# Kernel optimization log

Measured on AMD Instinct MI355X. Metric: run time of the kernel, lower is better.

Reference implementation:

```python
import jax, jax.numpy as jnp
import numpy as np

_SAMPLING_EPS = 1e-5


def setup_inputs() -> dict:
    key = jax.random.key(0)
    ks = jax.random.split(key, 7)
    N, V, H = 256, 128000, 200  # num_seqs, vocab_size, output-history length
    logits = jax.random.normal(ks[0], (N, V), dtype=jnp.float32)
    output_tokens = jax.random.randint(ks[1], (N, H), 0, V, dtype=jnp.int32)
    presence_penalties = jax.random.uniform(ks[2], (N,), jnp.float32, 0.0, 2.0)
    frequency_penalties = jax.random.uniform(ks[3], (N,), jnp.float32, 0.0, 2.0)
    temperatures = jax.random.uniform(ks[4], (N,), jnp.float32, 0.5, 1.5)
    top_ps = jax.random.uniform(ks[5], (N,), jnp.float32, 0.5, 1.0)
    top_ks = jax.random.randint(ks[6], (N,), 1, 1000, dtype=jnp.int32)
    return {
        "logits": logits,
        "presence_penalties": presence_penalties,
        "frequency_penalties": frequency_penalties,
        "temperatures": temperatures,
        "top_ps": top_ps,
        "output_tokens": output_tokens,
        "top_ks": top_ks,
    }


def reference(logits, presence_penalties, frequency_penalties, temperatures,
              top_ps, output_tokens, top_ks):
    N, V = logits.shape

    # ---- _apply_penalties: bincount of previously generated tokens per row ----
    rows = jnp.arange(N)[:, None]  # [N,1] broadcast against [N,H] token ids
    bin_counts = jnp.zeros((N, V), logits.dtype).at[rows, output_tokens].add(1.0)
    # rows are skipped when both penalties are < eps (original builds an index list)
    active = ((presence_penalties >= _SAMPLING_EPS) |
              (frequency_penalties >= _SAMPLING_EPS))[:, None]
    presence_mask = (bin_counts > 0.0).astype(logits.dtype)
    penalty = (frequency_penalties[:, None] * bin_counts
               + presence_penalties[:, None] * presence_mask)
    logits = logits - jnp.where(active, penalty, jnp.zeros((), logits.dtype))

    # ---- temperature scaling + softmax ----
    logits = logits / temperatures[:, None]
    probs = jax.nn.softmax(logits, axis=-1)

    # ---- _apply_top_p_top_k: sort desc, cumsum, mask, unsort ----
    probs_idx = jnp.argsort(-probs, axis=-1)                    # descending order
    probs_sort = jnp.take_along_axis(probs, probs_idx, axis=-1)
    probs_sum = jnp.cumsum(probs_sort, axis=-1)
    top_p_mask = (probs_sum - probs_sort) > top_ps[:, None]     # exclusive cumsum > p
    probs_sort = jnp.where(top_p_mask, 0.0, probs_sort)
    top_k_mask = jnp.arange(V, dtype=top_ks.dtype)[None, :] >= top_ks[:, None]
    probs_sort = jnp.where(top_k_mask, 0.0, probs_sort)
    inv_idx = jnp.argsort(probs_idx, axis=-1)                   # unsort permutation
    filtered_probs = jnp.take_along_axis(probs_sort, inv_idx, axis=-1)
    return filtered_probs
```

## Files before the change

kernel.cpp:

```cpp
#include <hip/hip_runtime.h>
#include <stdint.h>

#define NB 8192
#define BSHIFT 19
#define HS 512
#define HM 511
#define CAP 4096
#define CAP2 6144
#define PCAP 2048
#define NRB 2048
#define NT 1024
#define CAPTHR 1.75f

typedef unsigned long long ull;

__device__ __forceinline__ unsigned mono_u32(float x) {
    unsigned b = __float_as_uint(x);
    return (b & 0x80000000u) ? ~b : (b | 0x80000000u);
}
__device__ __forceinline__ float inv_mono(unsigned u) {
    unsigned b = (u & 0x80000000u) ? (u & 0x7fffffffu) : ~u;
    return __uint_as_float(b);
}

__device__ __forceinline__ float compute_x(float l, int cnt,
                                           float pres, float freq, float t) {
    float pen = __fadd_rn(__fmul_rn(freq, (float)cnt), (cnt > 0) ? pres : 0.0f);
    return __fdiv_rn(__fsub_rn(l, pen), t);
}

__global__ __launch_bounds__(NT) void k_fused(
    const float* __restrict__ logits, const int* __restrict__ tokens,
    const float* __restrict__ pres_v, const float* __restrict__ freq_v,
    const float* __restrict__ temps, const float* __restrict__ topp_v,
    const int* __restrict__ topk_v, int V, int H, float* __restrict__ out)
{
    __shared__ __align__(16) char smem[(32 + 16 + 8 + 4) * 1024];
    unsigned* hc = (unsigned*)smem;
    ull* skey = (ull*)smem;
    char* regB = smem + 32 * 1024;
    float* se = (float*)regB;
    ull* tmpc = (ull*)regB;
    char* regC = smem + 48 * 1024;
    unsigned* rh = (unsigned*)regC;
    unsigned* cbuf = (unsigned*)regB;
    char* regD = smem + 56 * 1024;
    int* hkey = (int*)regD;
    int* hval = (int*)(regD + 2 * 1024);
    __shared__ int wt_i[16];
    __shared__ float wt_f[16];
    __shared__ float esum_s, corr_s;
    __shared__ int bstar_s, lcnt_s, rb_s, pcnt_s, cap_s;

    int row = blockIdx.x, tid = threadIdx.x;
    int lane = tid & 63, wid = tid >> 6;
    for (int b = tid; b < NB; b += NT) hc[b] = 0u;
    if (tid == 0) {
        esum_s = 0.f; corr_s = 0.f; bstar_s = -1;
        lcnt_s = 0; rb_s = 0; pcnt_s = 0; cap_s = 0;
    }

    for (int i = tid; i < HS; i += NT) { hkey[i] = -1; hval[i] = 0; }
    __syncthreads();
    const int* trow = tokens + (size_t)row * H;
    for (int i = tid; i < H; i += NT) {
        int v = trow[i];
        unsigned h = ((unsigned)v * 2654435761u) >> 23;
        while (true) {
            int prev = atomicCAS(&hkey[h], -1, v);
            if (prev == -1 || prev == v) { atomicAdd(&hval[h], 1); break; }
            h = (h + 1) & HM;
        }
    }
    __syncthreads();

    float t = temps[row];
    float r = __fdiv_rn(1.0f, t);
    const float* lrow = logits + (size_t)row * V;
    const float4* l4p = (const float4*)lrow;
    float4* o4p = (float4*)(out + (size_t)row * V);
    const float4 z4 = make_float4(0.f, 0.f, 0.f, 0.f);
    int V4 = V >> 2;
    int ZITER = (V4 + NT - 1) / NT;
    int zc = 0;

    float es = 0.0f;
    int i = tid;
    for (; i + 7 * NT < V4; i += 8 * NT) {
        float4 arr[8];
#pragma unroll
        for (int q = 0; q < 8; ++q) arr[q] = l4p[i + q * NT];
#pragma unroll
        for (int q = 0; q < 8; ++q) {
            int vb = (i + q * NT) << 2;
#pragma unroll
            for (int j = 0; j < 4; ++j) {
                float l = (&arr[q].x)[j];
                float x = __fmul_rn(l, r);
                atomicAdd(&hc[mono_u32(x) >> BSHIFT], 1u);
                es += __expf(x);
                if (l >= CAPTHR) {
                    int pos = atomicAdd(&cap_s, 1);
                    if (pos < CAP2) cbuf[pos] = (unsigned)(vb + j);
                }
            }
        }
    }
    for (; i < V4; i += NT) {
        float4 A = l4p[i];
#pragma unroll
        for (int j = 0; j < 4; ++j) {
            float l = (&A.x)[j];
            float x = __fmul_rn(l, r);
            atomicAdd(&hc[mono_u32(x) >> BSHIFT], 1u);
            es += __expf(x);
            if (l >= CAPTHR) {
                int pos = atomicAdd(&cap_s, 1);
                if (pos < CAP2) cbuf[pos] = (unsigned)((i << 2) + j);
            }
        }
    }
    for (int v = (V4 << 2) + tid; v < V; v += NT) {
        float l = lrow[v];
        float x = __fmul_rn(l, r);
        atomicAdd(&hc[mono_u32(x) >> BSHIFT], 1u);
        es += __expf(x);
        if (l >= CAPTHR) {
            int pos = atomicAdd(&cap_s, 1);
            if (pos < CAP2) cbuf[pos] = (unsigned)v;
        }
    }
    for (int off = 32; off; off >>= 1) es += __shfl_down(es, off);
    if ((tid & 63) == 0) atomicAdd(&esum_s, es);
    __syncthreads();

    float pres = pres_v[row], freq = freq_v[row];
    int active = (pres >= 1e-5f) || (freq >= 1e-5f);
    float corr = 0.0f;
    if (active) {
        for (int s = tid; s < HS; s += NT) {
            int v = hkey[s];
            if (v >= 0) {
                int c = hval[s];
                float l = lrow[v];
                float x0 = __fmul_rn(l, r);
                float xp = compute_x(l, c, pres, freq, t);
                unsigned b0 = mono_u32(x0) >> BSHIFT;
                unsigned bp = mono_u32(xp) >> BSHIFT;
                if (b0 != bp) { atomicSub(&hc[b0], 1u); atomicAdd(&hc[bp], 1u); }
                corr += __expf(xp) - __expf(x0);
            }
        }
    }
    for (int off = 32; off; off >>= 1) corr += __shfl_down(corr, off);
    if ((tid & 63) == 0) atomicAdd(&corr_s, corr);
    __syncthreads();

    const int BPT = NB / NT;
    int base = tid * BPT;
    int acc = 0;
#pragma unroll
    for (int q = BPT - 1; q >= 0; --q) { acc += (int)hc[base + q]; hc[base + q] = (unsigned)acc; }
    int k = topk_v[row];
    {
        int v = acc;
#pragma unroll
        for (int off = 1; off < 64; off <<= 1) {
            int o = __shfl_down(v, off);
            if (lane + off < 64) v += o;
        }
        if (lane == 0) wt_i[wid] = v;
        __syncthreads();
        int above = v - acc;
#pragma unroll
        for (int w = 0; w < 16; ++w) if (w > wid) above += wt_i[w];
        int best = -1;
#pragma unroll
        for (int q = BPT - 1; q >= 0; --q)
            if ((int)hc[base + q] + above >= k) { best = base + q; break; }
        if (best >= 0) atomicMax(&bstar_s, best);
    }
    __syncthreads();
    int bst = bstar_s - 2;
    if (bst < 0) bst = 0;
    float Sp = esum_s + corr_s;
    int ccount = cap_s;
    __syncthreads();

    int lb = (int)(mono_u32(__fmul_rn(CAPTHR, r)) >> BSHIFT);
    bool skip_c = (ccount <= CAP2) && (lb < bst);

    if (skip_c) {
        unsigned myidx[6];
#pragma unroll
        for (int q = 0; q < 6; ++q) {
            int j2 = tid + q * NT;
            myidx[q] = (j2 < ccount) ? cbuf[j2] : 0xffffffffu;
        }
        float myl[6];
#pragma unroll
        for (int q = 0; q < 6; ++q)
            if (myidx[q] != 0xffffffffu) myl[q] = lrow[myidx[q]];
#pragma unroll
        for (int q = 0; q < 6; ++q) {
            if (myidx[q] != 0xffffffffu) {
                float l = myl[q];
                unsigned ua = mono_u32(__fmul_rn(l, r));
                if ((int)(ua >> BSHIFT) >= bst) {
                    unsigned ue = mono_u32(__fdiv_rn(l, t));
                    int pos = atomicAdd(&lcnt_s, 1);
                    if (pos < CAP)
                        skey[pos] = ((ull)ue << 32) | (unsigned)~myidx[q];
                }
            }
        }
    } else {
        i = tid;
        for (; i + 7 * NT < V4; i += 8 * NT) {
            float4 arr[8];
#pragma unroll
            for (int q = 0; q < 8; ++q) arr[q] = l4p[i + q * NT];
#pragma unroll
            for (int q = 0; q < 8; ++q) {
                int vb = (i + q * NT) << 2;
#pragma unroll
                for (int j = 0; j < 4; ++j) {
                    float l = (&arr[q].x)[j];
                    unsigned ua = mono_u32(__fmul_rn(l, r));
                    if ((int)(ua >> BSHIFT) >= bst) {
                        unsigned ue = mono_u32(__fdiv_rn(l, t));
                        int pos = atomicAdd(&lcnt_s, 1);
                        if (pos < CAP)
                            skey[pos] = ((ull)ue << 32) | (unsigned)~(unsigned)(vb + j);
                    }
                }
            }
        }
        for (; i < V4; i += NT) {
            float4 A = l4p[i];
#pragma unroll
            for (int j = 0; j < 4; ++j) {
                float l = (&A.x)[j];
                unsigned ua = mono_u32(__fmul_rn(l, r));
                if ((int)(ua >> BSHIFT) >= bst) {
                    unsigned ue = mono_u32(__fdiv_rn(l, t));
                    int pos = atomicAdd(&lcnt_s, 1);
                    if (pos < CAP)
                        skey[pos] = ((ull)ue << 32) | (unsigned)~(unsigned)((i << 2) + j);
                }
            }
        }
        for (int v = (V4 << 2) + tid; v < V; v += NT) {
            float l = lrow[v];
            unsigned ua = mono_u32(__fmul_rn(l, r));
            if ((int)(ua >> BSHIFT) >= bst) {
                unsigned ue = mono_u32(__fdiv_rn(l, t));
                int pos = atomicAdd(&lcnt_s, 1);
                if (pos < CAP)
                    skey[pos] = ((ull)ue << 32) | (unsigned)~(unsigned)v;
            }
        }
    }
    __syncthreads();
    int count = lcnt_s; if (count > CAP) count = CAP;

    if (active) {
        for (int j = tid; j < count; j += NT) {
            unsigned idx = ~(unsigned)(skey[j] & 0xffffffffull);
            unsigned h = (idx * 2654435761u) >> 23;
            int c = 0;
            while (true) {
                int kk = hkey[h];
                if (kk == (int)idx) { c = hval[h]; break; }
                if (kk == -1) break;
                h = (h + 1) & HM;
            }
            if (c > 0) {
                float xp = compute_x(lrow[idx], c, pres, freq, t);
                skey[j] = ((ull)mono_u32(xp) << 32) | (unsigned)~idx;
            }
        }
    }
    __syncthreads();
    for (int g = tid; g < NRB; g += NT) rh[g] = 0u;
    __syncthreads();
    int gmin = bst << 6;
    for (int j = tid; j < count; j += NT) {
        unsigned u = (unsigned)(skey[j] >> 32);
        int rel = (int)(u >> 13) - gmin;
        rel = rel < 0 ? 0 : (rel > NRB - 1 ? NRB - 1 : rel);
        atomicAdd(&rh[rel], 1u);
    }
    __syncthreads();
    {
        int b2i = tid * 2;
        int a2 = (int)rh[b2i + 1];
        rh[b2i + 1] = (unsigned)a2;
        a2 += (int)rh[b2i];
        rh[b2i] = (unsigned)a2;
        int v = a2;
#pragma unroll
        for (int off = 1; off < 64; off <<= 1) {
            int o = __shfl_down(v, off);
            if (lane + off < 64) v += o;
        }
        if (lane == 0) wt_i[wid] = v;
        __syncthreads();
        int above = v - a2;
#pragma unroll
        for (int w = 0; w < 16; ++w) if (w > wid) above += wt_i[w];
        int best = -1;
        if ((int)rh[b2i + 1] + above >= k) best = b2i + 1;
        else if ((int)rh[b2i] + above >= k) best = b2i;
        if (best >= 0) atomicMax(&rb_s, best);
    }
    __syncthreads();
    int rb = rb_s;
    for (int j = tid; j < count; j += NT) {
        unsigned u = (unsigned)(skey[j] >> 32);
        int rel = (int)(u >> 13) - gmin;
        rel = rel < 0 ? 0 : (rel > NRB - 1 ? NRB - 1 : rel);
        if (rel >= rb) {
            int pos = atomicAdd(&pcnt_s, 1);
            if (pos < PCAP) tmpc[pos] = skey[j];
        }
    }
    __syncthreads();
    int count2 = pcnt_s;
    if (count2 <= PCAP) {
        for (int j = tid; j < count2; j += NT) skey[j] = tmpc[j];
        count = count2;
    }
    __syncthreads();

    int m = 1; while (m < count) m <<= 1;
    for (int j = count + tid; j < m; j += NT) skey[j] = 0ull;
    __syncthreads();
    for (int kk = 2; kk <= m; kk <<= 1) {
        for (int jj = kk >> 1; jj > 0; jj >>= 1) {
            if (zc < ZITER) {
                int p = tid + zc * NT;
                if (p < V4) o4p[p] = z4;
                ++zc;
            }
            for (int i2 = tid; i2 < m; i2 += NT) {
                int ixj = i2 ^ jj;
                if (ixj > i2) {
                    ull A = skey[i2], B = skey[ixj];
                    bool up = ((i2 & kk) != 0);
                    if ((A > B) == up) { skey[i2] = B; skey[ixj] = A; }
                }
            }
            __syncthreads();
        }
    }
    for (; zc < ZITER; ++zc) {
        int p = tid + zc * NT;
        if (p < V4) o4p[p] = z4;
    }
    for (int v2 = (V4 << 2) + tid; v2 < V; v2 += NT)
        out[(size_t)row * V + v2] = 0.0f;

    for (int j = tid; j < CAP; j += NT)
        se[j] = (j < count) ? __expf(inv_mono((unsigned)(skey[j] >> 32))) : 0.0f;
    __syncthreads();
    int j0 = tid << 2;
    float e0 = se[j0], e1 = se[j0 + 1], e2 = se[j0 + 2], e3 = se[j0 + 3];
    float c0 = e0, c1 = c0 + e1, c2 = c1 + e2, c3 = c2 + e3;
    float vf = c3;
#pragma unroll
    for (int off = 1; off < 64; off <<= 1) {
        float o = __shfl_up(vf, off);
        if (lane >= off) vf += o;
    }
    if (lane == 63) wt_f[wid] = vf;
    __syncthreads();
    float pre = vf - c3;
#pragma unroll
    for (int w = 0; w < 16; ++w) if (w < wid) pre += wt_f[w];

    float pS = topp_v[row] * Sp;
    float inc[4] = {pre + c0, pre + c1, pre + c2, pre + c3};
    float ee[4] = {e0, e1, e2, e3};
#pragma unroll
    for (int q = 0; q < 4; ++q) {
        int j = j0 + q;
        if (j < count) {
            float e = ee[q];
            float excl = __fsub_rn(inc[q], e);
            if ((j < k) && (excl <= pS)) {
                unsigned idx = ~(unsigned)(skey[j] & 0xffffffffull);
                out[(size_t)row * V + idx] = __fdiv_rn(e, Sp);
            }
        }
    }
}

extern "C" void kernel_launch(void* const* d_in, const int* in_sizes, int n_in,
                              void* d_out, int out_size, void* d_ws, size_t ws_size,
                              hipStream_t stream) {
    const float* logits = (const float*)d_in[0];
    const float* pres   = (const float*)d_in[1];
    const float* freq   = (const float*)d_in[2];
    const float* temps  = (const float*)d_in[3];
    const float* topps  = (const float*)d_in[4];
    const int*   tokens = (const int*)d_in[5];
    const int*   topks  = (const int*)d_in[6];
    int N = in_sizes[1];
    int V = in_sizes[0] / N;
    int H = in_sizes[5] / N;
    float* out = (float*)d_out;

    k_fused<<<N, NT, 0, stream>>>(logits, tokens, pres, freq, temps, topps,
                                  topks, V, H, out);
}
```

Before: 282.2 us.

## Use LDS-only barriers and issue output zeroing up front before sort phase

Replaces __syncthreads with custom barriers that wait only on LDS counters, so outstanding global stores no longer stall each barrier. The interleaved zero-fill of the output row inside the bitonic sort loop is hoisted into a single loop before the histogram phase, and a full vmcnt barrier is added before the final scatter so the zeros land before the selected probabilities are written. The top-p load is hoisted early. This risks ordering bugs if any barrier actually needed the global-memory wait.

```diff
diff --git a/kernel.cpp b/kernel.cpp
--- a/kernel.cpp
+++ b/kernel.cpp
@@ -13,6 +13,17 @@
 #define CAPTHR 1.75f
 
 typedef unsigned long long ull;
+
+__device__ __forceinline__ void bar_lds() {
+    asm volatile("s_waitcnt lgkmcnt(0)" ::: "memory");
+    __builtin_amdgcn_s_barrier();
+    __builtin_amdgcn_sched_barrier(0);
+}
+__device__ __forceinline__ void bar_full() {
+    asm volatile("s_waitcnt vmcnt(0) lgkmcnt(0)" ::: "memory");
+    __builtin_amdgcn_s_barrier();
+    __builtin_amdgcn_sched_barrier(0);
+}
 
 __device__ __forceinline__ unsigned mono_u32(float x) {
     unsigned b = __float_as_uint(x);
@@ -75,6 +86,7 @@
     __syncthreads();
 
     float t = temps[row];
+    float topp = topp_v[row];
     float r = __fdiv_rn(1.0f, t);
     const float* lrow = logits + (size_t)row * V;
     const float4* l4p = (const float4*)lrow;
@@ -82,7 +94,6 @@
     const float4 z4 = make_float4(0.f, 0.f, 0.f, 0.f);
     int V4 = V >> 2;
     int ZITER = (V4 + NT - 1) / NT;
-    int zc = 0;
 
     float es = 0.0f;
     int i = tid;
@@ -281,9 +292,18 @@
             }
         }
     }
-    __syncthreads();
+
+#pragma unroll 1
+    for (int zc = 0; zc < ZITER; ++zc) {
+        int p = tid + zc * NT;
+        if (p < V4) o4p[p] = z4;
+    }
+    for (int v2 = (V4 << 2) + tid; v2 < V; v2 += NT)
+        out[(size_t)row * V + v2] = 0.0f;
+    bar_lds();
+
     for (int g = tid; g < NRB; g += NT) rh[g] = 0u;
-    __syncthreads();
+    bar_lds();
     int gmin = bst << 6;
     for (int j = tid; j < count; j += NT) {
         unsigned u = (unsigned)(skey[j] >> 32);
@@ -291,7 +311,7 @@
         rel = rel < 0 ? 0 : (rel > NRB - 1 ? NRB - 1 : rel);
         atomicAdd(&rh[rel], 1u);
     }
-    __syncthreads();
+    bar_lds();
     {
         int b2i = tid * 2;
         int a2 = (int)rh[b2i + 1];
@@ -305,7 +325,7 @@
             if (lane + off < 64) v += o;
         }
         if (lane == 0) wt_i[wid] = v;
-        __syncthreads();
+        bar_lds();
         int above = v - a2;
 #pragma unroll
         for (int w = 0; w < 16; ++w) if (w > wid) above += wt_i[w];
@@ -314,7 +334,7 @@
         else if ((int)rh[b2i] + above >= k) best = b2i;
         if (best >= 0) atomicMax(&rb_s, best);
     }
-    __syncthreads();
+    bar_lds();
     int rb = rb_s;
     for (int j = tid; j < count; j += NT) {
         unsigned u = (unsigned)(skey[j] >> 32);
@@ -325,24 +345,19 @@
             if (pos < PCAP) tmpc[pos] = skey[j];
         }
     }
-    __syncthreads();
+    bar_lds();
     int count2 = pcnt_s;
     if (count2 <= PCAP) {
         for (int j = tid; j < count2; j += NT) skey[j] = tmpc[j];
         count = count2;
     }
-    __syncthreads();
+    bar_lds();
 
     int m = 1; while (m < count) m <<= 1;
     for (int j = count + tid; j < m; j += NT) skey[j] = 0ull;
-    __syncthreads();
+    bar_lds();
     for (int kk = 2; kk <= m; kk <<= 1) {
         for (int jj = kk >> 1; jj > 0; jj >>= 1) {
-            if (zc < ZITER) {
-                int p = tid + zc * NT;
-                if (p < V4) o4p[p] = z4;
-                ++zc;
-            }
             for (int i2 = tid; i2 < m; i2 += NT) {
                 int ixj = i2 ^ jj;
                 if (ixj > i2) {
@@ -351,19 +366,13 @@
                     if ((A > B) == up) { skey[i2] = B; skey[ixj] = A; }
                 }
             }
-            __syncthreads();
-        }
-    }
-    for (; zc < ZITER; ++zc) {
-        int p = tid + zc * NT;
-        if (p < V4) o4p[p] = z4;
-    }
-    for (int v2 = (V4 << 2) + tid; v2 < V; v2 += NT)
-        out[(size_t)row * V + v2] = 0.0f;
+            bar_lds();
+        }
+    }
 
     for (int j = tid; j < CAP; j += NT)
         se[j] = (j < count) ? __expf(inv_mono((unsigned)(skey[j] >> 32))) : 0.0f;
-    __syncthreads();
+    bar_lds();
     int j0 = tid << 2;
     float e0 = se[j0], e1 = se[j0 + 1], e2 = se[j0 + 2], e3 = se[j0 + 3];
     float c0 = e0, c1 = c0 + e1, c2 = c1 + e2, c3 = c2 + e3;
@@ -374,12 +383,14 @@
         if (lane >= off) vf += o;
     }
     if (lane == 63) wt_f[wid] = vf;
-    __syncthreads();
+    bar_lds();
     float pre = vf - c3;
 #pragma unroll
     for (int w = 0; w < 16; ++w) if (w < wid) pre += wt_f[w];
 
-    float pS = topp_v[row] * Sp;
+    bar_full();
+
+    float pS = topp * Sp;
     float inc[4] = {pre + c0, pre + c1, pre + c2, pre + c3};
     float ee[4] = {e0, e1, e2, e3};
 #pragma unroll
```

Measured after the change: 290.9 us. 1.03x slower.

## Sort candidates in registers with wavefront shuffles and spread output zeroing

Applied to the files above, without the earlier changes.

When the candidate set fits in 2048 entries, the bitonic sort is padded to a fixed size of 2048. Each thread holds two keys in registers, and all stages with stride below 128 run through cross-lane shuffles, so they need no LDS traffic or block barriers. Only the strides of 128 and above still go through shared memory with barriers. The zeroing of the output row is now interleaved across the remaining barriers, and those barriers become a lighter LDS-only wait plus s_barrier. The trade-off is that small candidate counts now always sort a full 2048 keys, and the hand-written barrier relies on lgkmcnt ordering being sufficient.

```diff
diff --git a/kernel.cpp b/kernel.cpp
--- a/kernel.cpp
+++ b/kernel.cpp
@@ -14,6 +14,12 @@
 
 typedef unsigned long long ull;
 
+__device__ __forceinline__ void bar_lds() {
+    asm volatile("s_waitcnt lgkmcnt(0)" ::: "memory");
+    __builtin_amdgcn_s_barrier();
+    __builtin_amdgcn_sched_barrier(0);
+}
+
 __device__ __forceinline__ unsigned mono_u32(float x) {
     unsigned b = __float_as_uint(x);
     return (b & 0x80000000u) ? ~b : (b | 0x80000000u);
@@ -28,6 +34,25 @@
     float pen = __fadd_rn(__fmul_rn(freq, (float)cnt), (cnt > 0) ? pres : 0.0f);
     return __fdiv_rn(__fsub_rn(l, pen), t);
 }
+
+#define SHFL_STAGE(kk, jj) do {                                              \
+    int _s = (jj) >> 1;                                                      \
+    ull _pA = __shfl_xor(A, _s), _pB = __shfl_xor(B, _s);                    \
+    bool _keepmn = (((e0 & (jj)) == 0) == ((e0 & (kk)) != 0));               \
+    ull _mnA = (A < _pA) ? A : _pA, _mxA = (A < _pA) ? _pA : A;              \
+    ull _mnB = (B < _pB) ? B : _pB, _mxB = (B < _pB) ? _pB : B;              \
+    A = _keepmn ? _mnA : _mxA;  B = _keepmn ? _mnB : _mxB;                   \
+} while (0)
+#define PAIR_STAGE(kk) do {                                                  \
+    bool _up = ((e0 & (kk)) != 0);                                           \
+    ull _mn = (A < B) ? A : B, _mx = (A < B) ? B : A;                        \
+    A = _up ? _mn : _mx;  B = _up ? _mx : _mn;                               \
+} while (0)
+#define ZDRIB(nn) do {                                                       \
+    for (int _z = 0; _z < (nn) && zc < ZITER; ++_z) {                        \
+        int _p = tid + zc * NT; if (_p < V4) o4p[_p] = z4; ++zc;             \
+    }                                                                        \
+} while (0)
 
 __global__ __launch_bounds__(NT) void k_fused(
     const float* __restrict__ logits, const int* __restrict__ tokens,
@@ -75,6 +100,7 @@
     __syncthreads();
 
     float t = temps[row];
+    float topp = topp_v[row];
     float r = __fdiv_rn(1.0f, t);
     const float* lrow = logits + (size_t)row * V;
     const float4* l4p = (const float4*)lrow;
@@ -107,10 +133,10 @@
         }
     }
     for (; i < V4; i += NT) {
-        float4 A = l4p[i];
+        float4 A4 = l4p[i];
 #pragma unroll
         for (int j = 0; j < 4; ++j) {
-            float l = (&A.x)[j];
+            float l = (&A4.x)[j];
             float x = __fmul_rn(l, r);
             atomicAdd(&hc[mono_u32(x) >> BSHIFT], 1u);
             es += __expf(x);
@@ -237,10 +263,10 @@
             }
         }
         for (; i < V4; i += NT) {
-            float4 A = l4p[i];
+            float4 A4 = l4p[i];
 #pragma unroll
             for (int j = 0; j < 4; ++j) {
-                float l = (&A.x)[j];
+                float l = (&A4.x)[j];
                 unsigned ua = mono_u32(__fmul_rn(l, r));
                 if ((int)(ua >> BSHIFT) >= bst) {
                     unsigned ue = mono_u32(__fdiv_rn(l, t));
@@ -281,9 +307,10 @@
             }
         }
     }
-    __syncthreads();
+    ZDRIB(2); bar_lds();
+
     for (int g = tid; g < NRB; g += NT) rh[g] = 0u;
-    __syncthreads();
+    ZDRIB(2); bar_lds();
     int gmin = bst << 6;
     for (int j = tid; j < count; j += NT) {
         unsigned u = (unsigned)(skey[j] >> 32);
@@ -291,7 +318,7 @@
         rel = rel < 0 ? 0 : (rel > NRB - 1 ? NRB - 1 : rel);
         atomicAdd(&rh[rel], 1u);
     }
-    __syncthreads();
+    ZDRIB(2); bar_lds();
     {
         int b2i = tid * 2;
         int a2 = (int)rh[b2i + 1];
@@ -305,7 +332,7 @@
             if (lane + off < 64) v += o;
         }
         if (lane == 0) wt_i[wid] = v;
-        __syncthreads();
+        ZDRIB(2); bar_lds();
         int above = v - a2;
 #pragma unroll
         for (int w = 0; w < 16; ++w) if (w > wid) above += wt_i[w];
@@ -314,7 +341,7 @@
         else if ((int)rh[b2i] + above >= k) best = b2i;
         if (best >= 0) atomicMax(&rb_s, best);
     }
-    __syncthreads();
+    ZDRIB(2); bar_lds();
     int rb = rb_s;
     for (int j = tid; j < count; j += NT) {
         unsigned u = (unsigned)(skey[j] >> 32);
@@ -325,48 +352,77 @@
             if (pos < PCAP) tmpc[pos] = skey[j];
         }
     }
-    __syncthreads();
+    ZDRIB(2); bar_lds();
     int count2 = pcnt_s;
     if (count2 <= PCAP) {
         for (int j = tid; j < count2; j += NT) skey[j] = tmpc[j];
         count = count2;
     }
-    __syncthreads();
-
-    int m = 1; while (m < count) m <<= 1;
-    for (int j = count + tid; j < m; j += NT) skey[j] = 0ull;
-    __syncthreads();
-    for (int kk = 2; kk <= m; kk <<= 1) {
-        for (int jj = kk >> 1; jj > 0; jj >>= 1) {
-            if (zc < ZITER) {
-                int p = tid + zc * NT;
-                if (p < V4) o4p[p] = z4;
-                ++zc;
-            }
-            for (int i2 = tid; i2 < m; i2 += NT) {
-                int ixj = i2 ^ jj;
-                if (ixj > i2) {
-                    ull A = skey[i2], B = skey[ixj];
-                    bool up = ((i2 & kk) != 0);
-                    if ((A > B) == up) { skey[i2] = B; skey[ixj] = A; }
-                }
-            }
-            __syncthreads();
-        }
-    }
+    ZDRIB(2); bar_lds();
+
+    if (count <= PCAP) {
+        const int M = 2048;
+        for (int j = count + tid; j < M; j += NT) skey[j] = 0ull;
+        ZDRIB(2); bar_lds();
+        int e0 = (wid << 7) + (lane << 1);
+        ull A = skey[e0], B = skey[e0 + 1];
+        ZDRIB(2);
+        for (int kk = 2; kk <= 128; kk <<= 1) {
+            for (int jj = kk >> 1; jj >= 2; jj >>= 1) SHFL_STAGE(kk, jj);
+            PAIR_STAGE(kk);
+        }
+        for (int kk = 256; kk <= 2048; kk <<= 1) {
+            skey[e0] = A; skey[e0 + 1] = B;
+            ZDRIB(2); bar_lds();
+            for (int jj = kk >> 1; jj >= 128; jj >>= 1) {
+                for (int i2 = tid; i2 < M; i2 += NT) {
+                    int ixj = i2 ^ jj;
+                    if (ixj > i2) {
+                        ull X = skey[i2], Y = skey[ixj];
+                        bool up = ((i2 & kk) != 0);
+                        if ((X > Y) == up) { skey[i2] = Y; skey[ixj] = X; }
+                    }
+                }
+                ZDRIB(2); bar_lds();
+            }
+            A = skey[e0]; B = skey[e0 + 1];
+            for (int jj = 64; jj >= 2; jj >>= 1) SHFL_STAGE(kk, jj);
+            PAIR_STAGE(kk);
+        }
+        skey[e0] = A; skey[e0 + 1] = B;
+    } else {
+        int m = 1; while (m < count) m <<= 1;
+        for (int j = count + tid; j < m; j += NT) skey[j] = 0ull;
+        __syncthreads();
+        for (int kk = 2; kk <= m; kk <<= 1) {
+            for (int jj = kk >> 1; jj > 0; jj >>= 1) {
+                for (int i2 = tid; i2 < m; i2 += NT) {
+                    int ixj = i2 ^ jj;
+                    if (ixj > i2) {
+                        ull X = skey[i2], Y = skey[ixj];
+                        bool up = ((i2 & kk) != 0);
+                        if ((X > Y) == up) { skey[i2] = Y; skey[ixj] = X; }
+                    }
+                }
+                __syncthreads();
+            }
+        }
+    }
+
     for (; zc < ZITER; ++zc) {
         int p = tid + zc * NT;
         if (p < V4) o4p[p] = z4;
     }
     for (int v2 = (V4 << 2) + tid; v2 < V; v2 += NT)
         out[(size_t)row * V + v2] = 0.0f;
+    __syncthreads();
 
     for (int j = tid; j < CAP; j += NT)
         se[j] = (j < count) ? __expf(inv_mono((unsigned)(skey[j] >> 32))) : 0.0f;
     __syncthreads();
     int j0 = tid << 2;
-    float e0 = se[j0], e1 = se[j0 + 1], e2 = se[j0 + 2], e3 = se[j0 + 3];
-    float c0 = e0, c1 = c0 + e1, c2 = c1 + e2, c3 = c2 + e3;
+    float e0f = se[j0], e1 = se[j0 + 1], e2 = se[j0 + 2], e3 = se[j0 + 3];
+    float c0 = e0f, c1 = c0 + e1, c2 = c1 + e2, c3 = c2 + e3;
     float vf = c3;
 #pragma unroll
     for (int off = 1; off < 64; off <<= 1) {
@@ -379,9 +435,9 @@
 #pragma unroll
     for (int w = 0; w < 16; ++w) if (w < wid) pre += wt_f[w];
 
-    float pS = topp_v[row] * Sp;
+    float pS = topp * Sp;
     float inc[4] = {pre + c0, pre + c1, pre + c2, pre + c3};
-    float ee[4] = {e0, e1, e2, e3};
+    float ee[4] = {e0f, e1, e2, e3};
 #pragma unroll
     for (int q = 0; q < 4; ++q) {
         int j = j0 + q;
```

New measurement: 275.1 us. -2.5%, faster.
